# Performance work log

Hardware: AMD Instinct MI355X
Metric: run time of the kernel (lower is better)

The kernel has to match this reference:

```python
import jax, jax.numpy as jnp
import numpy as np

# Static configuration matching the selected code path:
#   mode='inject_subject', is_self_attn=True, layer_id='up_blocks.0' (inject layer, bank hit)
#   alpha = AlphaScheduler.alpha(step=20, total=50, 'up_blocks.0') = 0.8 * 0.6 = 0.48
B, L, D, H = 4, 1024, 1280, 20
DH = D // H  # 64
ALPHA = 0.48


def setup_inputs() -> dict:
    key = jax.random.key(0)
    ks = jax.random.split(key, 8)
    w = lambda k, shp: (jax.random.normal(k, shp, dtype=jnp.float32) * 0.02)
    return {
        "hidden_states": jax.random.normal(ks[0], (B, L, D), dtype=jnp.float32),
        "Wq": w(ks[1], (D, D)),
        "Wk": w(ks[2], (D, D)),
        "Wv": w(ks[3], (D, D)),
        "Wo": w(ks[4], (D, D)),
        "bo": jnp.zeros((D,), dtype=jnp.float32),
        # cached background K/V, stored after head_to_batch_dim -> [B*H, L_bg, DH]
        "K_bg": jax.random.normal(ks[5], (B * H, L, DH), dtype=jnp.float32),
        "V_bg": jax.random.normal(ks[6], (B * H, L, DH), dtype=jnp.float32),
    }


def _head_to_batch(x):  # [B, L, D] -> [B*H, L, DH]
    b, l, _ = x.shape
    return x.reshape(b, l, H, DH).transpose(0, 2, 1, 3).reshape(b * H, l, DH)


def _batch_to_head(x):  # [B*H, L, DH] -> [B, L, D]
    bh, l, _ = x.shape
    b = bh // H
    return x.reshape(b, H, l, DH).transpose(0, 2, 1, 3).reshape(b, l, D)


def reference(hidden_states, Wq, Wk, Wv, Wo, bo, K_bg, V_bg):
    # q/k/v projections (self-attention: k, v from hidden_states)
    q = _head_to_batch(hidden_states @ Wq)  # [B*H, L, DH]
    k = _head_to_batch(hidden_states @ Wk)
    v = _head_to_batch(hidden_states @ Wv)

    # inject_subject: concat cached background K/V scaled by alpha along kv-seq dim
    k = jnp.concatenate([k, ALPHA * K_bg], axis=1)  # [B*H, 2L, DH]
    v = jnp.concatenate([v, ALPHA * V_bg], axis=1)

    # _sdpa: q scaled by scale*sqrt(dh), SDPA divides by sqrt(dh) -> net factor `scale`
    scale = 1.0 / jnp.sqrt(jnp.asarray(DH, dtype=q.dtype))
    scores = jnp.einsum('bqd,bkd->bqk', q, k) * scale  # [B*H, L, 2L]
    probs = jax.nn.softmax(scores, axis=-1)
    context = jnp.einsum('bqk,bkd->bqd', probs, v)  # [B*H, L, DH]

    out = _batch_to_head(context) @ Wo + bo  # to_out[0] linear
    return out
```

## Files before the change

### kernel.cpp

```cpp
#include <hip/hip_runtime.h>
#include <hip/hip_bf16.h>

#define B_   4
#define L_   1024
#define D_   1280
#define H_   20
#define DH_  64
#define BH_  (B_*H_)
#define L2_  (2*L_)
#define ALPHA_ 0.48f

typedef __attribute__((ext_vector_type(8))) short short8;
typedef __attribute__((ext_vector_type(4))) float float4v;

__device__ __forceinline__ float bf2f(ushort u) {
    union { unsigned int i; float f; } v; v.i = ((unsigned int)u) << 16; return v.f;
}
__device__ __forceinline__ ushort f2bf(float f) {
    union { float f; unsigned int i; } v; v.f = f;
    unsigned int i = v.i;
    unsigned int r = i + 0x7FFF + ((i >> 16) & 1);
    return (ushort)(r >> 16);
}
__device__ __forceinline__ short8 pack8(float4 f0, float4 f1) {
    short8 o;
    o[0] = (short)f2bf(f0.x); o[1] = (short)f2bf(f0.y);
    o[2] = (short)f2bf(f0.z); o[3] = (short)f2bf(f0.w);
    o[4] = (short)f2bf(f1.x); o[5] = (short)f2bf(f1.y);
    o[6] = (short)f2bf(f1.z); o[7] = (short)f2bf(f1.w);
    return o;
}

__device__ __forceinline__ void async16(const void* g, void* l) {
    __builtin_amdgcn_global_load_lds(
        (__attribute__((address_space(1))) void*)g,
        (__attribute__((address_space(3))) void*)l, 16, 0, 0);
}

__global__ __launch_bounds__(256) void detect_dtype(const unsigned int* __restrict__ w,
                                                    int* __restrict__ flag) {
    __shared__ int cnt;
    if (threadIdx.x == 0) cnt = 0;
    __syncthreads();
    int local = 0;
    for (int i = threadIdx.x; i < 4096; i += 256) {
        unsigned e = (w[i] >> 7) & 0xFF;
        local += (e >= 100 && e <= 130) ? 1 : 0;
    }
    atomicAdd(&cnt, local);
    __syncthreads();
    if (threadIdx.x == 0) flag[0] = (cnt > 2048) ? 1 : 0;
}

__global__ __launch_bounds__(256) void prep(
    const void* __restrict__ w0, const void* __restrict__ w1,
    const void* __restrict__ w2, const void* __restrict__ w3,
    ushort* __restrict__ Wt,
    const void* __restrict__ Vbg, ushort* __restrict__ Vt,
    const void* __restrict__ X, ushort* __restrict__ Xb,
    const void* __restrict__ Kbg, ushort* __restrict__ Kcv,
    const int* __restrict__ flag) {
    bool is16 = flag[0] != 0;
    int bi = blockIdx.x, tid = threadIdx.x;
    if (bi < 2880) {
        const void* src; ushort* dst; int srcld, dstld; long sbase, dbase;
        if (bi < 1600) {
            int z = bi / 400, t4 = bi % 400;
            int by = t4 / 20, bx = t4 % 20;
            const void* srcs[4] = {w0, w1, w2, w3};
            src = srcs[z]; srcld = D_; dstld = D_;
            sbase = (long)(by * 64) * D_ + bx * 64;
            dst = Wt + (long)z * D_ * D_;
            dbase = (long)(bx * 64) * D_ + by * 64;
        } else {
            int j = bi - 1600;
            int bh = j >> 4, kt = j & 15;
            src = Vbg; srcld = DH_; dstld = L2_;
            sbase = ((long)bh * L_ + kt * 64) * DH_;
            dst = Vt;
            dbase = (long)bh * DH_ * L2_ + L_ + kt * 64;
        }
        __shared__ ushort t[64 * 72];
        int ldr = tid >> 3, ldc = (tid & 7) * 8;
#pragma unroll
        for (int i = 0; i < 2; i++) {
            int y = ldr + 32 * i;
            long idx = sbase + (long)y * srcld + ldc;
            short8 v;
            if (is16) v = *(const short8*)((const ushort*)src + idx);
            else {
                const float* s = (const float*)src;
                v = pack8(*(const float4*)&s[idx], *(const float4*)&s[idx + 4]);
            }
            *(short8*)&t[y * 72 + ldc] = v;
        }
        __syncthreads();
        int c = tid & 63, r0 = (tid >> 6) * 16;
#pragma unroll
        for (int i = 0; i < 2; i++) {
            short8 o;
#pragma unroll
            for (int j2 = 0; j2 < 8; j2++) o[j2] = (short)t[(r0 + i * 8 + j2) * 72 + c];
            *(short8*)&dst[dbase + (long)c * dstld + r0 + i * 8] = o;
        }
    } else if (bi < 5440) {
        if (is16) return;
        long i = ((long)(bi - 2880) * 256 + tid) * 8;
        const float* s = (const float*)X;
        *(short8*)&Xb[i] = pack8(*(const float4*)&s[i], *(const float4*)&s[i + 4]);
    } else {
        if (is16) return;
        long i = ((long)(bi - 5440) * 256 + tid) * 8;
        const float* s = (const float*)Kbg;
        *(short8*)&Kcv[i] = pack8(*(const float4*)&s[i], *(const float4*)&s[i + 4]);
    }
}

template<int BMt, int BNt, int WROWS, int WCOLS>
__global__ __launch_bounds__(256) void gemm_tpl(
    const ushort* __restrict__ A16, const void* __restrict__ Araw,
    const ushort* __restrict__ Bt,
    ushort* __restrict__ Qp, ushort* __restrict__ Kp, ushort* __restrict__ Vt,
    void* __restrict__ Out, const void* __restrict__ bo, int mode,
    const int* __restrict__ flag) {
    constexpr int MI = BMt / WROWS / 16;
    constexpr int NI = BNt / WCOLS / 16;
    __shared__ __align__(16) ushort Al[BMt * 32];
    __shared__ __align__(16) ushort Bl[BNt * 32];
    bool is16 = flag[0] != 0;
    const ushort* A = (mode == 0 && is16) ? (const ushort*)Araw : A16;
    int tid = threadIdx.x;
    int bx = blockIdx.x, by = blockIdx.y;
    int w = tid >> 6, lane = tid & 63, l15 = lane & 15, quad = lane >> 4;
    int wm = (w / WCOLS) * (BMt / WROWS);
    int wn = (w % WCOLS) * (BNt / WCOLS);
    float4v acc[MI][NI] = {};
    const int K = 1280;
    const ushort* Arow = A + (long)by * BMt * K + (tid >> 2) * K + (tid & 3) * 8;
    const ushort* Brow = Bt + (long)bx * BNt * K + (tid >> 2) * K + (tid & 3) * 8;

    for (int kb = 0; kb < K; kb += 32) {
        __syncthreads();
#pragma unroll
        for (int i = 0; i < BMt / 64; i++)
            async16(Arow + (long)i * 64 * K + kb, &Al[(i * 4 + w) * 512]);
#pragma unroll
        for (int i = 0; i < BNt / 64; i++)
            async16(Brow + (long)i * 64 * K + kb, &Bl[(i * 4 + w) * 512]);
        __syncthreads();
        short8 av[MI], bv[NI];
#pragma unroll
        for (int mi = 0; mi < MI; mi++)
            av[mi] = *(const short8*)&Al[(wm + mi * 16 + l15) * 32 + quad * 8];
#pragma unroll
        for (int ni = 0; ni < NI; ni++)
            bv[ni] = *(const short8*)&Bl[(wn + ni * 16 + l15) * 32 + quad * 8];
#pragma unroll
        for (int mi = 0; mi < MI; mi++)
#pragma unroll
            for (int ni = 0; ni < NI; ni++)
                acc[mi][ni] = __builtin_amdgcn_mfma_f32_16x16x32_bf16(av[mi], bv[ni], acc[mi][ni], 0, 0, 0);
    }

#pragma unroll
    for (int mi = 0; mi < MI; mi++) {
        int mloc = wm + mi * 16 + quad * 4;
#pragma unroll
        for (int ni = 0; ni < NI; ni++) {
            int nloc = wn + ni * 16 + l15;
#pragma unroll
            for (int r = 0; r < 4; r++) {
                int m = by * BMt + mloc + r;
                int n = bx * BNt + nloc;
                float v = acc[mi][ni][r];
                if (mode == 0) {
                    int which = n / 1280;
                    int np = n - which * 1280;
                    int b = m >> 10, l = m & 1023, h = np >> 6, dh = np & 63;
                    if (which == 0)
                        Qp[((long)(b * H_ + h) * L_ + l) * DH_ + dh] = f2bf(v * 0.125f);
                    else if (which == 1)
                        Kp[((long)(b * H_ + h) * L_ + l) * DH_ + dh] = f2bf(v);
                    else
                        Vt[((long)(b * H_ + h) * DH_ + dh) * L2_ + l] = f2bf(v);
                } else {
                    float bias = is16 ? bf2f(((const ushort*)bo)[n]) : ((const float*)bo)[n];
                    float o = v + bias;
                    if (is16) ((ushort*)Out)[(long)m * D_ + n] = f2bf(o);
                    else      ((float*)Out)[(long)m * D_ + n] = o;
                }
            }
        }
    }
}

#define FS 72

__global__ __launch_bounds__(256) void flash_attn(
    const ushort* __restrict__ Qp, const ushort* __restrict__ Kp,
    const void* __restrict__ KbgRaw, const ushort* __restrict__ Kcv,
    const ushort* __restrict__ Vt, ushort* __restrict__ Ctx,
    const int* __restrict__ flag) {
    __shared__ __align__(16) ushort Kl[64 * 64], Vl[64 * 64];
    __shared__ __align__(16) ushort Pl[128 * FS];
    const ushort* Kbg = flag[0] ? (const ushort*)KbgRaw : Kcv;
    int tid = threadIdx.x;
    int w = tid >> 6, lane = tid & 63, l15 = lane & 15, quad = lane >> 4;
    int bi = blockIdx.x;
    int bh = (bi & 7) * 10 + ((bi >> 3) % 10);
    int qt = bi / 80;

    const ushort* Qsrc = Qp + ((long)bh * L_ + qt * 128) * DH_;
#pragma unroll
    for (int i = 0; i < 4; i++) {
        int id = tid + 256 * i, r = id >> 3, c = id & 7;
        *(short8*)&Pl[r * FS + c * 8] = *(const short8*)&Qsrc[r * DH_ + c * 8];
    }
    __syncthreads();
    short8 aq[2][2];
#pragma unroll
    for (int mi = 0; mi < 2; mi++)
#pragma unroll
        for (int ks = 0; ks < 2; ks++)
            aq[mi][ks] = *(const short8*)&Pl[(w * 32 + mi * 16 + l15) * FS + ks * 32 + quad * 8];

    float rs[2][4] = {};
    float4v O[2][4] = {};
    const ushort* Vbh = Vt + (long)bh * DH_ * L2_;

    for (int kt = 0; kt < 32; kt++) {
        __syncthreads();
        const ushort* Ksrc = (kt < 16)
            ? Kp  + ((long)bh * L_ + kt * 64) * DH_
            : Kbg + ((long)bh * L_ + (kt - 16) * 64) * DH_;
#pragma unroll
        for (int i = 0; i < 2; i++) {
            int q = i * 4 + w;
            async16(&Ksrc[(long)lane * DH_ + q * 8], &Kl[q * 512]);
            async16(&Vbh[(long)lane * L2_ + kt * 64 + q * 8], &Vl[q * 512]);
        }
        __syncthreads();

        bool bg = (kt >= 16);
#pragma unroll
        for (int mi = 0; mi < 2; mi++) {
            float4v s[4] = {};
#pragma unroll
            for (int ks = 0; ks < 2; ks++)
#pragma unroll
                for (int nt = 0; nt < 4; nt++) {
                    short8 bk = *(const short8*)&Kl[((ks * 4 + quad) * 64 + nt * 16 + l15) * 8];
                    s[nt] = __builtin_amdgcn_mfma_f32_16x16x32_bf16(aq[mi][ks], bk, s[nt], 0, 0, 0);
                }
#pragma unroll
            for (int nt = 0; nt < 4; nt++)
#pragma unroll
                for (int r = 0; r < 4; r++) {
                    float sv = s[nt][r];
                    if (bg) sv *= ALPHA_;
                    float p = __expf(sv);
                    rs[mi][r] += p;
                    Pl[(w * 32 + mi * 16 + quad * 4 + r) * FS + nt * 16 + l15] =
                        f2bf(bg ? p * ALPHA_ : p);
                }
        }
        asm volatile("s_waitcnt lgkmcnt(0)\n" ::: "memory");
#pragma unroll
        for (int mi = 0; mi < 2; mi++)
#pragma unroll
            for (int ks = 0; ks < 2; ks++) {
                short8 ap = *(const short8*)&Pl[(w * 32 + mi * 16 + l15) * FS + ks * 32 + quad * 8];
#pragma unroll
                for (int nt = 0; nt < 4; nt++) {
                    short8 bv = *(const short8*)&Vl[((ks * 4 + quad) * 64 + nt * 16 + l15) * 8];
                    O[mi][nt] = __builtin_amdgcn_mfma_f32_16x16x32_bf16(ap, bv, O[mi][nt], 0, 0, 0);
                }
            }
    }
#pragma unroll
    for (int mi = 0; mi < 2; mi++)
#pragma unroll
        for (int r = 0; r < 4; r++) {
            float v = rs[mi][r];
            v += __shfl_xor(v, 1); v += __shfl_xor(v, 2);
            v += __shfl_xor(v, 4); v += __shfl_xor(v, 8);
            rs[mi][r] = v;
        }
    int b = bh / H_, h = bh % H_;
#pragma unroll
    for (int mi = 0; mi < 2; mi++)
#pragma unroll
        for (int r = 0; r < 4; r++) {
            float rcp = 1.f / rs[mi][r];
            int l = qt * 128 + w * 32 + mi * 16 + quad * 4 + r;
#pragma unroll
            for (int nt = 0; nt < 4; nt++)
                Ctx[(long)(b * L_ + l) * D_ + h * DH_ + nt * 16 + l15] =
                    f2bf(O[mi][nt][r] * rcp);
        }
}

extern "C" void kernel_launch(void* const* d_in, const int* in_sizes, int n_in,
                              void* d_out, int out_size, void* d_ws, size_t ws_size,
                              hipStream_t stream) {
    const void* X   = d_in[0];
    const void* Wq  = d_in[1];
    const void* Wk  = d_in[2];
    const void* Wv  = d_in[3];
    const void* Wo  = d_in[4];
    const void* bo  = d_in[5];
    const void* Kbg = d_in[6];
    const void* Vbg = d_in[7];

    char* ws = (char*)d_ws;
    size_t off = 0;
    auto alloc = [&](size_t bytes) {
        void* p = ws + off;
        off = (off + bytes + 255) & ~(size_t)255;
        return p;
    };
    int*    dflag = (int*)alloc(256);
    ushort* Wt    = (ushort*)alloc((size_t)4 * D_ * D_ * 2);
    ushort* Qp    = (ushort*)alloc((size_t)BH_ * L_ * DH_ * 2);
    ushort* Kp    = (ushort*)alloc((size_t)BH_ * L_ * DH_ * 2);
    ushort* Kcv   = (ushort*)alloc((size_t)BH_ * L_ * DH_ * 2);
    ushort* Vt    = (ushort*)alloc((size_t)BH_ * DH_ * L2_ * 2);
    ushort* Xb    = (ushort*)alloc((size_t)B_ * L_ * D_ * 2);
    ushort* Ctx   = Xb;
    ushort* Wqkv_t = Wt;
    ushort* Wo_t   = Wt + (size_t)3 * D_ * D_;

    dim3 tb(256);
    detect_dtype<<<1, tb, 0, stream>>>((const unsigned int*)Wq, dflag);
    prep<<<8000, tb, 0, stream>>>(Wq, Wk, Wv, Wo, Wt, Vbg, Vt, X, Xb, Kbg, Kcv, dflag);
    gemm_tpl<128, 128, 2, 2><<<dim3(30, 32), tb, 0, stream>>>(
        Xb, X, Wqkv_t, Qp, Kp, Vt, nullptr, nullptr, 0, dflag);
    flash_attn<<<dim3(640), tb, 0, stream>>>(Qp, Kp, Kbg, Kcv, Vt, Ctx, dflag);
    gemm_tpl<64, 128, 1, 4><<<dim3(10, 64), tb, 0, stream>>>(
        Ctx, nullptr, Wo_t, nullptr, nullptr, nullptr, d_out, bo, 1, dflag);
}
```

Baseline: 351.5 us.

## Load K/V fragments directly from global, transpose MFMA, pre-scale V_bg by alpha

The flash attention kernel drops its shared-memory K/V staging and the barriers around it. Each wave now loads its K and V MFMA fragments straight from global memory, and Q is read directly into registers. The MFMA operands are swapped so the score and output tiles come out transposed. That lets P and the context be written as packed 4-element bf16 stores, and the row-sum reduction becomes two shuffles. The alpha scaling of V_bg moves into the prep transpose, and the QKV GEMM epilogue writes V with packed stores. In exchange, each wave redundantly reads K/V from global/L2 instead of sharing it through LDS, and the ALPHA multiply on V_bg happens before bf16 rounding rather than after.

```diff
diff --git a/kernel.cpp b/kernel.cpp
--- a/kernel.cpp
+++ b/kernel.cpp
@@ -29,6 +29,13 @@
     o[4] = (short)f2bf(f1.x); o[5] = (short)f2bf(f1.y);
     o[6] = (short)f2bf(f1.z); o[7] = (short)f2bf(f1.w);
     return o;
+}
+__device__ __forceinline__ void pack4_store(ushort* dst, float a, float b, float c, float d) {
+    union { __hip_bfloat162 h; unsigned int u; } x, y;
+    x.h = __float22bfloat162_rn(make_float2(a, b));
+    y.h = __float22bfloat162_rn(make_float2(c, d));
+    uint2 v; v.x = x.u; v.y = y.u;
+    *(uint2*)dst = v;
 }
 
 __device__ __forceinline__ void async16(const void* g, void* l) {
@@ -63,6 +70,7 @@
     bool is16 = flag[0] != 0;
     int bi = blockIdx.x, tid = threadIdx.x;
     if (bi < 2880) {
+        bool doScale = (bi >= 1600);
         const void* src; ushort* dst; int srcld, dstld; long sbase, dbase;
         if (bi < 1600) {
             int z = bi / 400, t4 = bi % 400;
@@ -87,10 +95,22 @@
             int y = ldr + 32 * i;
             long idx = sbase + (long)y * srcld + ldc;
             short8 v;
-            if (is16) v = *(const short8*)((const ushort*)src + idx);
-            else {
+            if (is16) {
+                v = *(const short8*)((const ushort*)src + idx);
+                if (doScale) {
+#pragma unroll
+                    for (int j2 = 0; j2 < 8; j2++)
+                        v[j2] = (short)f2bf(ALPHA_ * bf2f((ushort)v[j2]));
+                }
+            } else {
                 const float* s = (const float*)src;
-                v = pack8(*(const float4*)&s[idx], *(const float4*)&s[idx + 4]);
+                float4 f0 = *(const float4*)&s[idx];
+                float4 f1 = *(const float4*)&s[idx + 4];
+                if (doScale) {
+                    f0.x *= ALPHA_; f0.y *= ALPHA_; f0.z *= ALPHA_; f0.w *= ALPHA_;
+                    f1.x *= ALPHA_; f1.y *= ALPHA_; f1.z *= ALPHA_; f1.w *= ALPHA_;
+                }
+                v = pack8(f0, f1);
             }
             *(short8*)&t[y * 72 + ldc] = v;
         }
@@ -162,30 +182,47 @@
                 acc[mi][ni] = __builtin_amdgcn_mfma_f32_16x16x32_bf16(av[mi], bv[ni], acc[mi][ni], 0, 0, 0);
     }
 
-#pragma unroll
-    for (int mi = 0; mi < MI; mi++) {
-        int mloc = wm + mi * 16 + quad * 4;
-#pragma unroll
-        for (int ni = 0; ni < NI; ni++) {
-            int nloc = wn + ni * 16 + l15;
-#pragma unroll
-            for (int r = 0; r < 4; r++) {
-                int m = by * BMt + mloc + r;
-                int n = bx * BNt + nloc;
-                float v = acc[mi][ni][r];
-                if (mode == 0) {
-                    int which = n / 1280;
-                    int np = n - which * 1280;
-                    int b = m >> 10, l = m & 1023, h = np >> 6, dh = np & 63;
-                    if (which == 0)
-                        Qp[((long)(b * H_ + h) * L_ + l) * DH_ + dh] = f2bf(v * 0.125f);
-                    else if (which == 1)
-                        Kp[((long)(b * H_ + h) * L_ + l) * DH_ + dh] = f2bf(v);
-                    else
-                        Vt[((long)(b * H_ + h) * DH_ + dh) * L2_ + l] = f2bf(v);
+    if (mode == 0) {
+        int which = bx / 10;
+#pragma unroll
+        for (int mi = 0; mi < MI; mi++) {
+            int m0 = by * BMt + wm + mi * 16 + quad * 4;
+            int b = m0 >> 10, l0 = m0 & 1023;
+#pragma unroll
+            for (int ni = 0; ni < NI; ni++) {
+                int n = bx * BNt + wn + ni * 16 + l15;
+                int np = n - which * 1280;
+                int h = np >> 6, dh = np & 63;
+                if (which == 0) {
+#pragma unroll
+                    for (int r = 0; r < 4; r++)
+                        Qp[((long)(b * H_ + h) * L_ + l0 + r) * DH_ + dh] =
+                            f2bf(acc[mi][ni][r] * 0.125f);
+                } else if (which == 1) {
+#pragma unroll
+                    for (int r = 0; r < 4; r++)
+                        Kp[((long)(b * H_ + h) * L_ + l0 + r) * DH_ + dh] =
+                            f2bf(acc[mi][ni][r]);
                 } else {
+                    pack4_store(&Vt[((long)(b * H_ + h) * DH_ + dh) * L2_ + l0],
+                                acc[mi][ni][0], acc[mi][ni][1],
+                                acc[mi][ni][2], acc[mi][ni][3]);
+                }
+            }
+        }
+    } else {
+#pragma unroll
+        for (int mi = 0; mi < MI; mi++) {
+            int mloc = wm + mi * 16 + quad * 4;
+#pragma unroll
+            for (int ni = 0; ni < NI; ni++) {
+                int nloc = wn + ni * 16 + l15;
+#pragma unroll
+                for (int r = 0; r < 4; r++) {
+                    int m = by * BMt + mloc + r;
+                    int n = bx * BNt + nloc;
                     float bias = is16 ? bf2f(((const ushort*)bo)[n]) : ((const float*)bo)[n];
-                    float o = v + bias;
+                    float o = acc[mi][ni][r] + bias;
                     if (is16) ((ushort*)Out)[(long)m * D_ + n] = f2bf(o);
                     else      ((float*)Out)[(long)m * D_ + n] = o;
                 }
@@ -201,7 +238,6 @@
     const void* __restrict__ KbgRaw, const ushort* __restrict__ Kcv,
     const ushort* __restrict__ Vt, ushort* __restrict__ Ctx,
     const int* __restrict__ flag) {
-    __shared__ __align__(16) ushort Kl[64 * 64], Vl[64 * 64];
     __shared__ __align__(16) ushort Pl[128 * FS];
     const ushort* Kbg = flag[0] ? (const ushort*)KbgRaw : Kcv;
     int tid = threadIdx.x;
@@ -210,94 +246,83 @@
     int bh = (bi & 7) * 10 + ((bi >> 3) % 10);
     int qt = bi / 80;
 
-    const ushort* Qsrc = Qp + ((long)bh * L_ + qt * 128) * DH_;
-#pragma unroll
-    for (int i = 0; i < 4; i++) {
-        int id = tid + 256 * i, r = id >> 3, c = id & 7;
-        *(short8*)&Pl[r * FS + c * 8] = *(const short8*)&Qsrc[r * DH_ + c * 8];
-    }
-    __syncthreads();
     short8 aq[2][2];
+    const ushort* Qb = Qp + ((long)bh * L_ + qt * 128 + w * 32) * DH_;
 #pragma unroll
     for (int mi = 0; mi < 2; mi++)
 #pragma unroll
         for (int ks = 0; ks < 2; ks++)
-            aq[mi][ks] = *(const short8*)&Pl[(w * 32 + mi * 16 + l15) * FS + ks * 32 + quad * 8];
-
-    float rs[2][4] = {};
+            aq[mi][ks] = *(const short8*)&Qb[(mi * 16 + l15) * DH_ + ks * 32 + quad * 8];
+
+    float rs[2] = {0.f, 0.f};
     float4v O[2][4] = {};
-    const ushort* Vbh = Vt + (long)bh * DH_ * L2_;
+    const ushort* Vb = Vt + (long)bh * DH_ * L2_;
+    int prow = (w * 32 + l15) * FS;
 
     for (int kt = 0; kt < 32; kt++) {
-        __syncthreads();
         const ushort* Ksrc = (kt < 16)
             ? Kp  + ((long)bh * L_ + kt * 64) * DH_
             : Kbg + ((long)bh * L_ + (kt - 16) * 64) * DH_;
-#pragma unroll
-        for (int i = 0; i < 2; i++) {
-            int q = i * 4 + w;
-            async16(&Ksrc[(long)lane * DH_ + q * 8], &Kl[q * 512]);
-            async16(&Vbh[(long)lane * L2_ + kt * 64 + q * 8], &Vl[q * 512]);
-        }
-        __syncthreads();
-
         bool bg = (kt >= 16);
+        short8 bk[2][4], bv[2][4];
+#pragma unroll
+        for (int ks = 0; ks < 2; ks++)
+#pragma unroll
+            for (int nt = 0; nt < 4; nt++) {
+                bk[ks][nt] = *(const short8*)&Ksrc[(nt * 16 + l15) * DH_ + ks * 32 + quad * 8];
+                bv[ks][nt] = *(const short8*)&Vb[(long)(nt * 16 + l15) * L2_ + kt * 64 + ks * 32 + quad * 8];
+            }
 #pragma unroll
         for (int mi = 0; mi < 2; mi++) {
             float4v s[4] = {};
 #pragma unroll
             for (int ks = 0; ks < 2; ks++)
 #pragma unroll
-                for (int nt = 0; nt < 4; nt++) {
-                    short8 bk = *(const short8*)&Kl[((ks * 4 + quad) * 64 + nt * 16 + l15) * 8];
-                    s[nt] = __builtin_amdgcn_mfma_f32_16x16x32_bf16(aq[mi][ks], bk, s[nt], 0, 0, 0);
-                }
-#pragma unroll
-            for (int nt = 0; nt < 4; nt++)
+                for (int nt = 0; nt < 4; nt++)
+                    s[nt] = __builtin_amdgcn_mfma_f32_16x16x32_bf16(bk[ks][nt], aq[mi][ks], s[nt], 0, 0, 0);
+#pragma unroll
+            for (int nt = 0; nt < 4; nt++) {
+                float p[4];
 #pragma unroll
                 for (int r = 0; r < 4; r++) {
                     float sv = s[nt][r];
                     if (bg) sv *= ALPHA_;
-                    float p = __expf(sv);
-                    rs[mi][r] += p;
-                    Pl[(w * 32 + mi * 16 + quad * 4 + r) * FS + nt * 16 + l15] =
-                        f2bf(bg ? p * ALPHA_ : p);
-                }
+                    p[r] = __expf(sv);
+                    rs[mi] += p[r];
+                }
+                pack4_store(&Pl[prow + mi * 16 * FS + nt * 16 + quad * 4],
+                            p[0], p[1], p[2], p[3]);
+            }
         }
         asm volatile("s_waitcnt lgkmcnt(0)\n" ::: "memory");
 #pragma unroll
         for (int mi = 0; mi < 2; mi++)
 #pragma unroll
             for (int ks = 0; ks < 2; ks++) {
-                short8 ap = *(const short8*)&Pl[(w * 32 + mi * 16 + l15) * FS + ks * 32 + quad * 8];
-#pragma unroll
-                for (int nt = 0; nt < 4; nt++) {
-                    short8 bv = *(const short8*)&Vl[((ks * 4 + quad) * 64 + nt * 16 + l15) * 8];
-                    O[mi][nt] = __builtin_amdgcn_mfma_f32_16x16x32_bf16(ap, bv, O[mi][nt], 0, 0, 0);
-                }
-            }
-    }
-#pragma unroll
-    for (int mi = 0; mi < 2; mi++)
-#pragma unroll
-        for (int r = 0; r < 4; r++) {
-            float v = rs[mi][r];
-            v += __shfl_xor(v, 1); v += __shfl_xor(v, 2);
-            v += __shfl_xor(v, 4); v += __shfl_xor(v, 8);
-            rs[mi][r] = v;
-        }
+                short8 ap = *(const short8*)&Pl[prow + mi * 16 * FS + ks * 32 + quad * 8];
+#pragma unroll
+                for (int nt = 0; nt < 4; nt++)
+                    O[mi][nt] = __builtin_amdgcn_mfma_f32_16x16x32_bf16(bv[ks][nt], ap, O[mi][nt], 0, 0, 0);
+            }
+    }
+    float rcp[2];
+#pragma unroll
+    for (int mi = 0; mi < 2; mi++) {
+        float v = rs[mi];
+        v += __shfl_xor(v, 16);
+        v += __shfl_xor(v, 32);
+        rcp[mi] = 1.f / v;
+    }
     int b = bh / H_, h = bh % H_;
 #pragma unroll
-    for (int mi = 0; mi < 2; mi++)
-#pragma unroll
-        for (int r = 0; r < 4; r++) {
-            float rcp = 1.f / rs[mi][r];
-            int l = qt * 128 + w * 32 + mi * 16 + quad * 4 + r;
-#pragma unroll
-            for (int nt = 0; nt < 4; nt++)
-                Ctx[(long)(b * L_ + l) * D_ + h * DH_ + nt * 16 + l15] =
-                    f2bf(O[mi][nt][r] * rcp);
-        }
+    for (int mi = 0; mi < 2; mi++) {
+        long l = qt * 128 + w * 32 + mi * 16 + l15;
+#pragma unroll
+        for (int nt = 0; nt < 4; nt++)
+            pack4_store(&Ctx[(long)(b * L_ + l) * D_ + h * DH_ + nt * 16 + quad * 4],
+                        O[mi][nt][0] * rcp[mi], O[mi][nt][1] * rcp[mi],
+                        O[mi][nt][2] * rcp[mi], O[mi][nt][3] * rcp[mi]);
+    }
 }
 
 extern "C" void kernel_launch(void* const* d_in, const int* in_sizes, int n_in,
```

Measured after the change: 421.4 us. +19.9%, slower.
